# Kernel tuning notes

Measured on AMD Instinct MI355X. Metric: run time of the kernel, lower is better.

## Reference

```python
import jax, jax.numpy as jnp
import numpy as np

VX, VY = 0.16, 0.16
PC_RANGE = (0.0, -39.68, -3.0, 69.12, 39.68, 1.0)
X_OFFSET = VX / 2.0 + PC_RANGE[0]
Y_OFFSET = VY / 2.0 + PC_RANGE[1]
BN_EPS = 1e-3


def setup_inputs() -> dict:
    key = jax.random.key(0)
    k1, k2, k3, k4, k5, k6 = jax.random.split(key, 6)
    P, N, C_IN, C_AUG, C_OUT = 30000, 32, 4, 9, 64
    inputs = jax.random.normal(k1, (P, N, C_IN), dtype=jnp.float32)
    num_points = jnp.maximum(jax.random.randint(k2, (P,), 0, N, dtype=jnp.int32), 1)
    coords = jax.random.randint(k3, (P, 4), 0, 432, dtype=jnp.int32)
    # PFN layer params: Linear(9->64, no bias), BatchNorm1d(64) affine params
    W = jax.random.normal(k4, (C_AUG, C_OUT), dtype=jnp.float32) * (1.0 / np.sqrt(C_AUG))
    gamma = jnp.ones((C_OUT,), dtype=jnp.float32) + 0.1 * jax.random.normal(k5, (C_OUT,), dtype=jnp.float32)
    beta = 0.1 * jax.random.normal(k6, (C_OUT,), dtype=jnp.float32)
    return {"inputs": inputs, "num_points": num_points, "coords": coords,
            "W": W, "gamma": gamma, "beta": beta}


def reference(inputs, num_points, coords, W, gamma, beta):
    # inputs: (P, N, 4); num_points: (P,); coords: (P, 4) = (batch, z, y, x)
    P, N, _ = inputs.shape
    dtype = inputs.dtype
    npf = num_points.astype(dtype)

    # cluster offsets: per-pillar mean of xyz (sum over all N slots / num_points, as in source)
    points_mean = inputs[:, :, :3].sum(axis=1, keepdims=True) / npf[:, None, None]
    f_cluster = inputs[:, :, :3] - points_mean  # (P, N, 3)

    # center offsets w.r.t. pillar center
    cx = coords[:, 3].astype(dtype)[:, None] * VX + X_OFFSET  # (P, 1)
    cy = coords[:, 2].astype(dtype)[:, None] * VY + Y_OFFSET
    f_center = jnp.stack([inputs[:, :, 0] - cx, inputs[:, :, 1] - cy], axis=-1)  # (P, N, 2)

    feats = jnp.concatenate([inputs, f_cluster, f_center], axis=-1)  # (P, N, 9)

    # zero out padding points
    mask = (jnp.arange(N)[None, :] < num_points[:, None]).astype(dtype)[:, :, None]
    feats = feats * mask

    # PFNLayer: linear -> BatchNorm1d (training-mode batch stats over P*N) -> ReLU -> max over points
    x = jnp.einsum('pnc,cd->pnd', feats, W)  # (P, N, 64)
    mean = x.mean(axis=(0, 1))
    var = jnp.mean(jnp.square(x - mean), axis=(0, 1))  # biased, as torch BN
    x = (x - mean) * jax.lax.rsqrt(var + BN_EPS) * gamma + beta
    x = jax.nn.relu(x)
    return x.max(axis=1)  # (P, 64)
```

## Files before the change

### kernel.cpp

```cpp
#include <hip/hip_runtime.h>
#include <math.h>


#define NSLOT 32
#define NCH 64

static constexpr float kVX = 0.16f, kVY = 0.16f;
static constexpr float kXOff = 0.08f;
static constexpr float kYOff = 0.08f - 39.68f;
static constexpr float kEps = 1e-3f;
static constexpr float kNegInf = -3.402823466e38f;

typedef int sv16 __attribute__((ext_vector_type(16)));
typedef int sv8 __attribute__((ext_vector_type(8)));
union U16 { sv16 v; float f[16]; };
union U8  { sv8 v;  float f[8]; int i[8]; };

__device__ __forceinline__ const float* uptr(const float* p) {
    unsigned long long v = (unsigned long long)p;
    unsigned lo = __builtin_amdgcn_readfirstlane((unsigned)v);
    unsigned hi = __builtin_amdgcn_readfirstlane((unsigned)(v >> 32));
    return (const float*)(((unsigned long long)hi << 32) | lo);
}

__global__ __launch_bounds__(256) void k_stats(const float* __restrict__ in,
                                               const int* __restrict__ npts,
                                               const int* __restrict__ coords,
                                               float* __restrict__ part,
                                               float* __restrict__ meta, int P) {
    const int tid = threadIdx.x;
    const int lane = tid & 63;
    const int wv = tid >> 6;
    const int sub = lane & 3;
    const int pi = blockIdx.x * 64 + wv * 16 + (lane >> 2);
    const bool valid = pi < P;

    float T0 = 0.f, T1 = 0.f, T2 = 0.f;
    float S0 = 0.f, S1 = 0.f, S2 = 0.f, S3 = 0.f;
    float Q[10];
#pragma unroll
    for (int i = 0; i < 10; ++i) Q[i] = 0.f;
    float cx = 0.f, cy = 0.f, npf = 1.f;
    int np = 1;

    if (valid) {
        np = npts[pi];
        np = np < 1 ? 1 : (np > NSLOT ? NSLOT : np);
        npf = (float)np;
        const int4 cd = *reinterpret_cast<const int4*>(coords + (size_t)pi * 4);
        cx = (float)cd.w * kVX + kXOff;
        cy = (float)cd.z * kVY + kYOff;
        const float* bp = in + (size_t)pi * 128 + sub * 4;
#pragma unroll
        for (int k = 0; k < 8; ++k) {
            const float4 u = *reinterpret_cast<const float4*>(bp + k * 16);
            const int slot = sub + k * 4;
            T0 += u.x; T1 += u.y; T2 += u.z;
            const bool m = slot < np;
            const float ax = m ? u.x : 0.f, ay = m ? u.y : 0.f;
            const float az = m ? u.z : 0.f, aw = m ? u.w : 0.f;
            S0 += ax; S1 += ay; S2 += az; S3 += aw;
            Q[0] += ax * u.x; Q[1] += ax * u.y; Q[2] += ax * u.z; Q[3] += ax * u.w;
            Q[4] += ay * u.y; Q[5] += ay * u.z; Q[6] += ay * u.w;
            Q[7] += az * u.z; Q[8] += az * u.w;
            Q[9] += aw * u.w;
        }
    }

#define QUADR(v) { v += __shfl_xor(v, 1); v += __shfl_xor(v, 2); }
    QUADR(T0) QUADR(T1) QUADR(T2)
    QUADR(S0) QUADR(S1) QUADR(S2) QUADR(S3)
#pragma unroll
    for (int i = 0; i < 10; ++i) QUADR(Q[i])
#undef QUADR

    float acc[54];
#pragma unroll
    for (int i = 0; i < 54; ++i) acc[i] = 0.f;

    if (valid && sub == 0) {
        const float inv = 1.0f / npf;
        const float mx = T0 * inv, my = T1 * inv, mz = T2 * inv;
        if (meta) {
            *reinterpret_cast<float4*>(meta + (size_t)pi * 8) =
                make_float4(mx, my, mz, __int_as_float(np));
            *reinterpret_cast<float4*>(meta + (size_t)pi * 8 + 4) =
                make_float4(cx, cy, 0.f, 0.f);
        }
        const float AS[9] = {S0, S1, S2, S3, S0, S1, S2, S0, S1};
        const float b9[9] = {0.f, 0.f, 0.f, 0.f, -mx, -my, -mz, -cx, -cy};
        const int r9[9] = {0, 1, 2, 3, 0, 1, 2, 0, 1};
        float Qm[4][4];
        Qm[0][0] = Q[0]; Qm[0][1] = Q[1]; Qm[0][2] = Q[2]; Qm[0][3] = Q[3];
        Qm[1][0] = Q[1]; Qm[1][1] = Q[4]; Qm[1][2] = Q[5]; Qm[1][3] = Q[6];
        Qm[2][0] = Q[2]; Qm[2][1] = Q[5]; Qm[2][2] = Q[7]; Qm[2][3] = Q[8];
        Qm[3][0] = Q[3]; Qm[3][1] = Q[6]; Qm[3][2] = Q[8]; Qm[3][3] = Q[9];
#pragma unroll
        for (int i = 0; i < 9; ++i) acc[i] = AS[i] + npf * b9[i];
        int k = 9;
#pragma unroll
        for (int i = 0; i < 9; ++i)
#pragma unroll
            for (int j = i; j < 9; ++j) {
                acc[k] = Qm[r9[i]][r9[j]] + AS[i] * b9[j] + b9[i] * AS[j]
                         + npf * b9[i] * b9[j];
                ++k;
            }
    }

#pragma unroll
    for (int i = 0; i < 54; ++i) {
        acc[i] += __shfl_xor(acc[i], 4);
        acc[i] += __shfl_xor(acc[i], 8);
        acc[i] += __shfl_xor(acc[i], 16);
        acc[i] += __shfl_xor(acc[i], 32);
    }

    __shared__ float red[4][54];
    if (lane == 0) {
#pragma unroll
        for (int i = 0; i < 54; ++i) red[wv][i] = acc[i];
    }
    __syncthreads();
    if (tid < 54) {
        part[(size_t)blockIdx.x * 64 + tid] =
            red[0][tid] + red[1][tid] + red[2][tid] + red[3][tid];
    }
}

__global__ __launch_bounds__(1024) void k_mid(const float* __restrict__ part,
                                              const float* __restrict__ W,
                                              const float* __restrict__ gamma,
                                              const float* __restrict__ beta,
                                              float* __restrict__ fold,
                                              int nb, int P) {
    __shared__ float sred[16][64];
    __shared__ float ssum[64];
    const int tid = threadIdx.x;
    const int e = tid & 63;
    const int grp = tid >> 6;
    float v0 = 0.f, v1 = 0.f, v2 = 0.f, v3 = 0.f;
    int i = grp;
    for (; i + 48 < nb; i += 64) {
        v0 += part[(size_t)i * 64 + e];
        v1 += part[(size_t)(i + 16) * 64 + e];
        v2 += part[(size_t)(i + 32) * 64 + e];
        v3 += part[(size_t)(i + 48) * 64 + e];
    }
    for (; i < nb; i += 16) v0 += part[(size_t)i * 64 + e];
    sred[grp][e] = (v0 + v1) + (v2 + v3);
    __syncthreads();
    if (tid < 64) {
        float v = 0.f;
#pragma unroll
        for (int g = 0; g < 16; ++g) v += sred[g][tid];
        ssum[tid] = v;
    }
    __syncthreads();

    if (tid < 64) {
        const int d = tid;
        float Wc[9];
#pragma unroll
        for (int c = 0; c < 9; ++c) Wc[c] = W[c * NCH + d];
        const float invPN = 1.0f / ((float)P * (float)NSLOT);
        float mean = 0.f;
#pragma unroll
        for (int c = 0; c < 9; ++c) mean += ssum[c] * Wc[c];
        mean *= invPN;
        float e2 = 0.f;
        int k = 9;
#pragma unroll
        for (int i2 = 0; i2 < 9; ++i2)
#pragma unroll
            for (int j = i2; j < 9; ++j) {
                const float coef = (i2 == j) ? 1.f : 2.f;
                e2 += coef * ssum[k] * Wc[i2] * Wc[j];
                ++k;
            }
        e2 *= invPN;
        const float var = e2 - mean * mean;
        const float s = gamma[d] * rsqrtf(var + kEps);
        const float t = beta[d] - mean * s;
        fold[0 * 64 + d] = s * (Wc[0] + Wc[4] + Wc[7]);
        fold[1 * 64 + d] = s * (Wc[1] + Wc[5] + Wc[8]);
        fold[2 * 64 + d] = s * (Wc[2] + Wc[6]);
        fold[3 * 64 + d] = s * Wc[3];
        fold[4 * 64 + d] = s * Wc[4];
        fold[5 * 64 + d] = s * Wc[5];
        fold[6 * 64 + d] = s * Wc[6];
        fold[7 * 64 + d] = s * Wc[7];
        fold[8 * 64 + d] = s * Wc[8];
        fold[9 * 64 + d] = t;
    }
}

__device__ __forceinline__ float dot4(const float4 u, float V0, float V1,
                                      float V2, float V3, float c0) {
    return fmaf(u.x, V0, fmaf(u.y, V1, fmaf(u.z, V2, fmaf(u.w, V3, c0))));
}

template <bool MEANS>
__global__ __launch_bounds__(256) void k_out(const float* __restrict__ in,
                                             const int* __restrict__ npts,
                                             const int* __restrict__ coords,
                                             const float* __restrict__ fold,
                                             const float* __restrict__ meta,
                                             float* __restrict__ out, int P) {
    const int tid = threadIdx.x;
    const int lane = tid & 63;
    const int wv = tid >> 6;
    const int gwave = blockIdx.x * 4 + wv;
    const int nwave = gridDim.x * 4;

    float F[10];
#pragma unroll
    for (int j = 0; j < 10; ++j) F[j] = fold[j * 64 + lane];
    const float V0 = F[0], V1 = F[1], V2 = F[2], V3 = F[3];
    const float sW4 = F[4], sW5 = F[5], sW6 = F[6], sW7 = F[7], sW8 = F[8];
    const float t = F[9];

    if (MEANS) {
        for (int p = gwave; p < P; p += nwave) {
            const float* up = uptr(in + (size_t)p * 128);
            const float* mp = uptr(meta + (size_t)p * 8);
            U8 m; U16 g0, g1, g2, g3;
            asm volatile(
                "s_load_dwordx8 %0, %2, 0x0\n\t"
                "s_load_dwordx16 %1, %3, 0x0"
                : "=s"(m.v), "=s"(g0.v) : "s"(mp), "s"(up));
            asm volatile(
                "s_load_dwordx16 %0, %2, 0x40\n\t"
                "s_load_dwordx16 %1, %2, 0x80"
                : "=s"(g1.v), "=s"(g2.v) : "s"(up));
            asm volatile(
                "s_load_dwordx16 %0, %1, 0xc0"
                : "=s"(g3.v) : "s"(up));
            asm volatile("s_waitcnt lgkmcnt(0)" ::: "memory");
            __builtin_amdgcn_sched_barrier(0);

            const int np = m.i[3];
            const float c0 = t - fmaf(m.f[0], sW4, fmaf(m.f[1], sW5,
                                 fmaf(m.f[2], sW6, fmaf(m.f[4], sW7,
                                      m.f[5] * sW8))));
            float y0 = t, y1 = t, y2 = t, y3 = t;
#define SLOT4(G, B) { \
            const float z0 = fmaf(G.f[0], V0, fmaf(G.f[1], V1, \
                               fmaf(G.f[2], V2, fmaf(G.f[3], V3, c0)))); \
            const float z1 = fmaf(G.f[4], V0, fmaf(G.f[5], V1, \
                               fmaf(G.f[6], V2, fmaf(G.f[7], V3, c0)))); \
            const float z2 = fmaf(G.f[8], V0, fmaf(G.f[9], V1, \
                               fmaf(G.f[10], V2, fmaf(G.f[11], V3, c0)))); \
            const float z3 = fmaf(G.f[12], V0, fmaf(G.f[13], V1, \
                               fmaf(G.f[14], V2, fmaf(G.f[15], V3, c0)))); \
            y0 = fmaxf(y0, ((B) + 0 < np) ? z0 : t); \
            y1 = fmaxf(y1, ((B) + 1 < np) ? z1 : t); \
            y2 = fmaxf(y2, ((B) + 2 < np) ? z2 : t); \
            y3 = fmaxf(y3, ((B) + 3 < np) ? z3 : t); }

            SLOT4(g0, 0)
            SLOT4(g1, 4)
            if (np > 8) {
                SLOT4(g2, 8)
                SLOT4(g3, 12)
            }
            if (np > 16) {
                U16 h0, h1, h2, h3;
                asm volatile(
                    "s_load_dwordx16 %0, %2, 0x100\n\t"
                    "s_load_dwordx16 %1, %2, 0x140"
                    : "=s"(h0.v), "=s"(h1.v) : "s"(up));
                asm volatile(
                    "s_load_dwordx16 %0, %2, 0x180\n\t"
                    "s_load_dwordx16 %1, %2, 0x1c0"
                    : "=s"(h2.v), "=s"(h3.v) : "s"(up));
                asm volatile("s_waitcnt lgkmcnt(0)" ::: "memory");
                __builtin_amdgcn_sched_barrier(0);
                SLOT4(h0, 16)
                SLOT4(h1, 20)
                SLOT4(h2, 24)
                SLOT4(h3, 28)
            }
#undef SLOT4
            out[(size_t)p * NCH + lane] =
                fmaxf(fmaxf(fmaxf(y0, y1), fmaxf(y2, y3)), 0.f);
        }
    } else {
        __shared__ float lds[4][128];
        for (int p = gwave; p < P; p += nwave) {
            const float2 g = *reinterpret_cast<const float2*>(in + (size_t)p * 128 + lane * 2);
            int np = npts[p];
            np = np < 1 ? 1 : (np > NSLOT ? NSLOT : np);
            const bool ev = !(lane & 1);
            float px = ev ? g.x : 0.f;
            float py = ev ? g.y : 0.f;
            float pz = ev ? 0.f : g.x;
#pragma unroll
            for (int m = 1; m < 64; m <<= 1) {
                px += __shfl_xor(px, m);
                py += __shfl_xor(py, m);
                pz += __shfl_xor(pz, m);
            }
            const float npf = (float)np;
            const float mx = px / npf, my = py / npf, mz = pz / npf;
            const int4 cd = *reinterpret_cast<const int4*>(coords + (size_t)p * 4);
            const float cx = (float)cd.w * kVX + kXOff;
            const float cy = (float)cd.z * kVY + kYOff;
            const float c0 = t - (mx * sW4 + my * sW5 + mz * sW6 + cx * sW7 + cy * sW8);
            *reinterpret_cast<float2*>(&lds[wv][lane * 2]) = g;
            const float* L = lds[wv];
            float y0 = (np < NSLOT) ? t : kNegInf;
            float y1 = kNegInf;
            int n = 0;
            for (; n + 2 <= np; n += 2) {
                const float4 u0 = *reinterpret_cast<const float4*>(L + n * 4);
                const float4 u1 = *reinterpret_cast<const float4*>(L + n * 4 + 4);
                y0 = fmaxf(y0, dot4(u0, V0, V1, V2, V3, c0));
                y1 = fmaxf(y1, dot4(u1, V0, V1, V2, V3, c0));
            }
            if (n < np) {
                const float4 u0 = *reinterpret_cast<const float4*>(L + n * 4);
                y0 = fmaxf(y0, dot4(u0, V0, V1, V2, V3, c0));
            }
            out[(size_t)p * NCH + lane] = fmaxf(fmaxf(y0, y1), 0.f);
        }
    }
}

extern "C" void kernel_launch(void* const* d_in, const int* in_sizes, int n_in,
                              void* d_out, int out_size, void* d_ws, size_t ws_size,
                              hipStream_t stream) {
    const float* in = (const float*)d_in[0];
    const int* npts = (const int*)d_in[1];
    const int* coords = (const int*)d_in[2];
    const float* W = (const float*)d_in[3];
    const float* gamma = (const float*)d_in[4];
    const float* beta = (const float*)d_in[5];
    float* out = (float*)d_out;
    float* ws = (float*)d_ws;
    const int P = in_sizes[1];

    const int nb = (P + 63) / 64;
    const size_t foff = (size_t)nb * 64;
    const size_t moff = (foff + 640 + 63) & ~(size_t)63;
    float* part = ws;
    float* fold = ws + foff;
    const bool means = ws_size >= (moff + 8 * (size_t)P) * sizeof(float);
    float* meta = means ? (ws + moff) : nullptr;

    k_stats<<<nb, 256, 0, stream>>>(in, npts, coords, part, meta, P);
    k_mid<<<1, 1024, 0, stream>>>(part, W, gamma, beta, fold, nb, P);
    if (means) {
        k_out<true><<<2048, 256, 0, stream>>>(in, npts, coords, fold, meta, out, P);
    } else {
        k_out<false><<<2048, 256, 0, stream>>>(in, npts, coords, fold, meta, out, P);
    }
}
```

Before: 31.29 us.

## Fuse stats reduction into output kernel, dropping the single-block mid kernel

Removes the separate single-block k_mid launch. Each output block now redundantly reduces all partial statistics itself and folds the BatchNorm scale and shift into per-channel weights. The output grid changes from 2048 persistent blocks to one block per 32 pillars, and the LDS fallback path without meta is removed. This saves one launch and the serial single-block gap, but every one of about 938 blocks rereads the full part buffer (about 120 KB), adding redundant L2 traffic and latency before each block's main loop.

```diff
diff --git a/kernel.cpp b/kernel.cpp
--- a/kernel.cpp
+++ b/kernel.cpp
@@ -9,7 +9,6 @@
 static constexpr float kXOff = 0.08f;
 static constexpr float kYOff = 0.08f - 39.68f;
 static constexpr float kEps = 1e-3f;
-static constexpr float kNegInf = -3.402823466e38f;
 
 typedef int sv16 __attribute__((ext_vector_type(16)));
 typedef int sv8 __attribute__((ext_vector_type(8)));
@@ -81,12 +80,10 @@
     if (valid && sub == 0) {
         const float inv = 1.0f / npf;
         const float mx = T0 * inv, my = T1 * inv, mz = T2 * inv;
-        if (meta) {
-            *reinterpret_cast<float4*>(meta + (size_t)pi * 8) =
-                make_float4(mx, my, mz, __int_as_float(np));
-            *reinterpret_cast<float4*>(meta + (size_t)pi * 8 + 4) =
-                make_float4(cx, cy, 0.f, 0.f);
-        }
+        *reinterpret_cast<float4*>(meta + (size_t)pi * 8) =
+            make_float4(mx, my, mz, __int_as_float(np));
+        *reinterpret_cast<float4*>(meta + (size_t)pi * 8 + 4) =
+            make_float4(cx, cy, 0.f, 0.f);
         const float AS[9] = {S0, S1, S2, S3, S0, S1, S2, S0, S1};
         const float b9[9] = {0.f, 0.f, 0.f, 0.f, -mx, -my, -mz, -cx, -cy};
         const int r9[9] = {0, 1, 2, 3, 0, 1, 2, 0, 1};
@@ -128,47 +125,58 @@
     }
 }
 
-__global__ __launch_bounds__(1024) void k_mid(const float* __restrict__ part,
-                                              const float* __restrict__ W,
-                                              const float* __restrict__ gamma,
-                                              const float* __restrict__ beta,
-                                              float* __restrict__ fold,
-                                              int nb, int P) {
-    __shared__ float sred[16][64];
+__global__ __launch_bounds__(256) void k_out(const float* __restrict__ in,
+                                             const float* __restrict__ W,
+                                             const float* __restrict__ gamma,
+                                             const float* __restrict__ beta,
+                                             const float* __restrict__ part,
+                                             const float* __restrict__ meta,
+                                             float* __restrict__ out,
+                                             int P, int nb) {
+    __shared__ float sred[4][64];
     __shared__ float ssum[64];
     const int tid = threadIdx.x;
-    const int e = tid & 63;
-    const int grp = tid >> 6;
-    float v0 = 0.f, v1 = 0.f, v2 = 0.f, v3 = 0.f;
-    int i = grp;
-    for (; i + 48 < nb; i += 64) {
-        v0 += part[(size_t)i * 64 + e];
-        v1 += part[(size_t)(i + 16) * 64 + e];
-        v2 += part[(size_t)(i + 32) * 64 + e];
-        v3 += part[(size_t)(i + 48) * 64 + e];
-    }
-    for (; i < nb; i += 16) v0 += part[(size_t)i * 64 + e];
-    sred[grp][e] = (v0 + v1) + (v2 + v3);
-    __syncthreads();
-    if (tid < 64) {
-        float v = 0.f;
-#pragma unroll
-        for (int g = 0; g < 16; ++g) v += sred[g][tid];
-        ssum[tid] = v;
-    }
-    __syncthreads();
-
-    if (tid < 64) {
-        const int d = tid;
-        float Wc[9];
-#pragma unroll
-        for (int c = 0; c < 9; ++c) Wc[c] = W[c * NCH + d];
-        const float invPN = 1.0f / ((float)P * (float)NSLOT);
-        float mean = 0.f;
-#pragma unroll
-        for (int c = 0; c < 9; ++c) mean += ssum[c] * Wc[c];
-        mean *= invPN;
-        float e2 = 0.f;
+    const int lane = tid & 63;
+    const int wv = tid >> 6;
+
+    {
+        const int e = tid & 63;
+        const int grp = tid >> 6;
+        const int rpc = (nb + 3) >> 2;
+        const int i0 = grp * rpc;
+        const int i1 = min(i0 + rpc, nb);
+        float v0 = 0.f, v1 = 0.f, v2 = 0.f, v3 = 0.f;
+        float v4 = 0.f, v5 = 0.f, v6 = 0.f, v7 = 0.f;
+        int i = i0;
+        for (; i + 8 <= i1; i += 8) {
+            v0 += part[(size_t)(i + 0) * 64 + e];
+            v1 += part[(size_t)(i + 1) * 64 + e];
+            v2 += part[(size_t)(i + 2) * 64 + e];
+            v3 += part[(size_t)(i + 3) * 64 + e];
+            v4 += part[(size_t)(i + 4) * 64 + e];
+            v5 += part[(size_t)(i + 5) * 64 + e];
+            v6 += part[(size_t)(i + 6) * 64 + e];
+            v7 += part[(size_t)(i + 7) * 64 + e];
+        }
+        for (; i < i1; ++i) v0 += part[(size_t)i * 64 + e];
+        sred[grp][e] = ((v0 + v1) + (v2 + v3)) + ((v4 + v5) + (v6 + v7));
+        __syncthreads();
+        if (tid < 64)
+            ssum[tid] = sred[0][tid] + sred[1][tid] + sred[2][tid] + sred[3][tid];
+        __syncthreads();
+    }
+
+    const int d = lane;
+    float Wc[9];
+#pragma unroll
+    for (int c = 0; c < 9; ++c) Wc[c] = W[c * NCH + d];
+    const float invPN = 1.0f / ((float)P * (float)NSLOT);
+    float mean = 0.f;
+#pragma unroll
+    for (int c = 0; c < 9; ++c) mean += ssum[c] * Wc[c];
+    mean *= invPN;
+    float e2 = 0.f;
+    {
         int k = 9;
 #pragma unroll
         for (int i2 = 0; i2 < 9; ++i2)
@@ -178,152 +186,84 @@
                 e2 += coef * ssum[k] * Wc[i2] * Wc[j];
                 ++k;
             }
-        e2 *= invPN;
-        const float var = e2 - mean * mean;
-        const float s = gamma[d] * rsqrtf(var + kEps);
-        const float t = beta[d] - mean * s;
-        fold[0 * 64 + d] = s * (Wc[0] + Wc[4] + Wc[7]);
-        fold[1 * 64 + d] = s * (Wc[1] + Wc[5] + Wc[8]);
-        fold[2 * 64 + d] = s * (Wc[2] + Wc[6]);
-        fold[3 * 64 + d] = s * Wc[3];
-        fold[4 * 64 + d] = s * Wc[4];
-        fold[5 * 64 + d] = s * Wc[5];
-        fold[6 * 64 + d] = s * Wc[6];
-        fold[7 * 64 + d] = s * Wc[7];
-        fold[8 * 64 + d] = s * Wc[8];
-        fold[9 * 64 + d] = t;
-    }
-}
-
-__device__ __forceinline__ float dot4(const float4 u, float V0, float V1,
-                                      float V2, float V3, float c0) {
-    return fmaf(u.x, V0, fmaf(u.y, V1, fmaf(u.z, V2, fmaf(u.w, V3, c0))));
-}
-
-template <bool MEANS>
-__global__ __launch_bounds__(256) void k_out(const float* __restrict__ in,
-                                             const int* __restrict__ npts,
-                                             const int* __restrict__ coords,
-                                             const float* __restrict__ fold,
-                                             const float* __restrict__ meta,
-                                             float* __restrict__ out, int P) {
-    const int tid = threadIdx.x;
-    const int lane = tid & 63;
-    const int wv = tid >> 6;
-    const int gwave = blockIdx.x * 4 + wv;
-    const int nwave = gridDim.x * 4;
-
-    float F[10];
-#pragma unroll
-    for (int j = 0; j < 10; ++j) F[j] = fold[j * 64 + lane];
-    const float V0 = F[0], V1 = F[1], V2 = F[2], V3 = F[3];
-    const float sW4 = F[4], sW5 = F[5], sW6 = F[6], sW7 = F[7], sW8 = F[8];
-    const float t = F[9];
-
-    if (MEANS) {
-        for (int p = gwave; p < P; p += nwave) {
-            const float* up = uptr(in + (size_t)p * 128);
-            const float* mp = uptr(meta + (size_t)p * 8);
-            U8 m; U16 g0, g1, g2, g3;
+    }
+    e2 *= invPN;
+    const float var = e2 - mean * mean;
+    const float s = gamma[d] * rsqrtf(var + kEps);
+    const float t = beta[d] - mean * s;
+    const float V0 = s * (Wc[0] + Wc[4] + Wc[7]);
+    const float V1 = s * (Wc[1] + Wc[5] + Wc[8]);
+    const float V2 = s * (Wc[2] + Wc[6]);
+    const float V3 = s * Wc[3];
+    const float sW4 = s * Wc[4], sW5 = s * Wc[5], sW6 = s * Wc[6];
+    const float sW7 = s * Wc[7], sW8 = s * Wc[8];
+
+    const int p0 = blockIdx.x * 32;
+    const int qmax = min(32, P - p0);
+    for (int q = wv; q < qmax; q += 4) {
+        const int p = p0 + q;
+        const float* up = uptr(in + (size_t)p * 128);
+        const float* mp = uptr(meta + (size_t)p * 8);
+        U8 m; U16 g0, g1, g2, g3;
+        asm volatile(
+            "s_load_dwordx8 %0, %2, 0x0\n\t"
+            "s_load_dwordx16 %1, %3, 0x0"
+            : "=s"(m.v), "=s"(g0.v) : "s"(mp), "s"(up));
+        asm volatile(
+            "s_load_dwordx16 %0, %2, 0x40\n\t"
+            "s_load_dwordx16 %1, %2, 0x80"
+            : "=s"(g1.v), "=s"(g2.v) : "s"(up));
+        asm volatile(
+            "s_load_dwordx16 %0, %1, 0xc0"
+            : "=s"(g3.v) : "s"(up));
+        asm volatile("s_waitcnt lgkmcnt(0)" ::: "memory");
+        __builtin_amdgcn_sched_barrier(0);
+
+        const int np = m.i[3];
+        const float c0 = t - fmaf(m.f[0], sW4, fmaf(m.f[1], sW5,
+                             fmaf(m.f[2], sW6, fmaf(m.f[4], sW7,
+                                  m.f[5] * sW8))));
+        float y0 = t, y1 = t, y2 = t, y3 = t;
+#define SLOT4(G, B) { \
+        const float z0 = fmaf(G.f[0], V0, fmaf(G.f[1], V1, \
+                           fmaf(G.f[2], V2, fmaf(G.f[3], V3, c0)))); \
+        const float z1 = fmaf(G.f[4], V0, fmaf(G.f[5], V1, \
+                           fmaf(G.f[6], V2, fmaf(G.f[7], V3, c0)))); \
+        const float z2 = fmaf(G.f[8], V0, fmaf(G.f[9], V1, \
+                           fmaf(G.f[10], V2, fmaf(G.f[11], V3, c0)))); \
+        const float z3 = fmaf(G.f[12], V0, fmaf(G.f[13], V1, \
+                           fmaf(G.f[14], V2, fmaf(G.f[15], V3, c0)))); \
+        y0 = fmaxf(y0, ((B) + 0 < np) ? z0 : t); \
+        y1 = fmaxf(y1, ((B) + 1 < np) ? z1 : t); \
+        y2 = fmaxf(y2, ((B) + 2 < np) ? z2 : t); \
+        y3 = fmaxf(y3, ((B) + 3 < np) ? z3 : t); }
+
+        SLOT4(g0, 0)
+        SLOT4(g1, 4)
+        if (np > 8) {
+            SLOT4(g2, 8)
+            SLOT4(g3, 12)
+        }
+        if (np > 16) {
+            U16 h0, h1, h2, h3;
             asm volatile(
-                "s_load_dwordx8 %0, %2, 0x0\n\t"
-                "s_load_dwordx16 %1, %3, 0x0"
-                : "=s"(m.v), "=s"(g0.v) : "s"(mp), "s"(up));
+                "s_load_dwordx16 %0, %2, 0x100\n\t"
+                "s_load_dwordx16 %1, %2, 0x140"
+                : "=s"(h0.v), "=s"(h1.v) : "s"(up));
             asm volatile(
-                "s_load_dwordx16 %0, %2, 0x40\n\t"
-                "s_load_dwordx16 %1, %2, 0x80"
-                : "=s"(g1.v), "=s"(g2.v) : "s"(up));
-            asm volatile(
-                "s_load_dwordx16 %0, %1, 0xc0"
-                : "=s"(g3.v) : "s"(up));
+                "s_load_dwordx16 %0, %2, 0x180\n\t"
+                "s_load_dwordx16 %1, %2, 0x1c0"
+                : "=s"(h2.v), "=s"(h3.v) : "s"(up));
             asm volatile("s_waitcnt lgkmcnt(0)" ::: "memory");
             __builtin_amdgcn_sched_barrier(0);
-
-            const int np = m.i[3];
-            const float c0 = t - fmaf(m.f[0], sW4, fmaf(m.f[1], sW5,
-                                 fmaf(m.f[2], sW6, fmaf(m.f[4], sW7,
-                                      m.f[5] * sW8))));
-            float y0 = t, y1 = t, y2 = t, y3 = t;
-#define SLOT4(G, B) { \
-            const float z0 = fmaf(G.f[0], V0, fmaf(G.f[1], V1, \
-                               fmaf(G.f[2], V2, fmaf(G.f[3], V3, c0)))); \
-            const float z1 = fmaf(G.f[4], V0, fmaf(G.f[5], V1, \
-                               fmaf(G.f[6], V2, fmaf(G.f[7], V3, c0)))); \
-            const float z2 = fmaf(G.f[8], V0, fmaf(G.f[9], V1, \
-                               fmaf(G.f[10], V2, fmaf(G.f[11], V3, c0)))); \
-            const float z3 = fmaf(G.f[12], V0, fmaf(G.f[13], V1, \
-                               fmaf(G.f[14], V2, fmaf(G.f[15], V3, c0)))); \
-            y0 = fmaxf(y0, ((B) + 0 < np) ? z0 : t); \
-            y1 = fmaxf(y1, ((B) + 1 < np) ? z1 : t); \
-            y2 = fmaxf(y2, ((B) + 2 < np) ? z2 : t); \
-            y3 = fmaxf(y3, ((B) + 3 < np) ? z3 : t); }
-
-            SLOT4(g0, 0)
-            SLOT4(g1, 4)
-            if (np > 8) {
-                SLOT4(g2, 8)
-                SLOT4(g3, 12)
-            }
-            if (np > 16) {
-                U16 h0, h1, h2, h3;
-                asm volatile(
-                    "s_load_dwordx16 %0, %2, 0x100\n\t"
-                    "s_load_dwordx16 %1, %2, 0x140"
-                    : "=s"(h0.v), "=s"(h1.v) : "s"(up));
-                asm volatile(
-                    "s_load_dwordx16 %0, %2, 0x180\n\t"
-                    "s_load_dwordx16 %1, %2, 0x1c0"
-                    : "=s"(h2.v), "=s"(h3.v) : "s"(up));
-                asm volatile("s_waitcnt lgkmcnt(0)" ::: "memory");
-                __builtin_amdgcn_sched_barrier(0);
-                SLOT4(h0, 16)
-                SLOT4(h1, 20)
-                SLOT4(h2, 24)
-                SLOT4(h3, 28)
-            }
+            SLOT4(h0, 16)
+            SLOT4(h1, 20)
+            SLOT4(h2, 24)
+            SLOT4(h3, 28)
+        }
 #undef SLOT4
-            out[(size_t)p * NCH + lane] =
-                fmaxf(fmaxf(fmaxf(y0, y1), fmaxf(y2, y3)), 0.f);
-        }
-    } else {
-        __shared__ float lds[4][128];
-        for (int p = gwave; p < P; p += nwave) {
-            const float2 g = *reinterpret_cast<const float2*>(in + (size_t)p * 128 + lane * 2);
-            int np = npts[p];
-            np = np < 1 ? 1 : (np > NSLOT ? NSLOT : np);
-            const bool ev = !(lane & 1);
-            float px = ev ? g.x : 0.f;
-            float py = ev ? g.y : 0.f;
-            float pz = ev ? 0.f : g.x;
-#pragma unroll
-            for (int m = 1; m < 64; m <<= 1) {
-                px += __shfl_xor(px, m);
-                py += __shfl_xor(py, m);
-                pz += __shfl_xor(pz, m);
-            }
-            const float npf = (float)np;
-            const float mx = px / npf, my = py / npf, mz = pz / npf;
-            const int4 cd = *reinterpret_cast<const int4*>(coords + (size_t)p * 4);
-            const float cx = (float)cd.w * kVX + kXOff;
-            const float cy = (float)cd.z * kVY + kYOff;
-            const float c0 = t - (mx * sW4 + my * sW5 + mz * sW6 + cx * sW7 + cy * sW8);
-            *reinterpret_cast<float2*>(&lds[wv][lane * 2]) = g;
-            const float* L = lds[wv];
-            float y0 = (np < NSLOT) ? t : kNegInf;
-            float y1 = kNegInf;
-            int n = 0;
-            for (; n + 2 <= np; n += 2) {
-                const float4 u0 = *reinterpret_cast<const float4*>(L + n * 4);
-                const float4 u1 = *reinterpret_cast<const float4*>(L + n * 4 + 4);
-                y0 = fmaxf(y0, dot4(u0, V0, V1, V2, V3, c0));
-                y1 = fmaxf(y1, dot4(u1, V0, V1, V2, V3, c0));
-            }
-            if (n < np) {
-                const float4 u0 = *reinterpret_cast<const float4*>(L + n * 4);
-                y0 = fmaxf(y0, dot4(u0, V0, V1, V2, V3, c0));
-            }
-            out[(size_t)p * NCH + lane] = fmaxf(fmaxf(y0, y1), 0.f);
-        }
+        out[(size_t)p * NCH + lane] =
+            fmaxf(fmaxf(fmaxf(y0, y1), fmaxf(y2, y3)), 0.f);
     }
 }
 
@@ -341,18 +281,11 @@
     const int P = in_sizes[1];
 
     const int nb = (P + 63) / 64;
-    const size_t foff = (size_t)nb * 64;
-    const size_t moff = (foff + 640 + 63) & ~(size_t)63;
+    const size_t moff = ((size_t)nb * 64 + 63) & ~(size_t)63;
     float* part = ws;
-    float* fold = ws + foff;
-    const bool means = ws_size >= (moff + 8 * (size_t)P) * sizeof(float);
-    float* meta = means ? (ws + moff) : nullptr;
+    float* meta = ws + moff;
 
     k_stats<<<nb, 256, 0, stream>>>(in, npts, coords, part, meta, P);
-    k_mid<<<1, 1024, 0, stream>>>(part, W, gamma, beta, fold, nb, P);
-    if (means) {
-        k_out<true><<<2048, 256, 0, stream>>>(in, npts, coords, fold, meta, out, P);
-    } else {
-        k_out<false><<<2048, 256, 0, stream>>>(in, npts, coords, fold, meta, out, P);
-    }
-}
+    const int ob = (P + 31) / 32;
+    k_out<<<ob, 256, 0, stream>>>(in, W, gamma, beta, part, meta, out, P, nb);
+}
```

After: 35.66 us. 1.14x slower.

## Replace shuffle reduction with LDS transpose and specialize slot masking

Applied to the files above, without the earlier changes.

In k_stats, the 54-value cross-lane shuffle reduction is replaced by writing each pillar's accumulators to a padded LDS matrix and summing columns across threads. In k_out, the fallback non-meta path is removed, so the meta workspace is always assumed present. Groups of four slots that are fully valid now skip the per-slot np comparison and select, and partial groups past np are skipped. This trims shuffle traffic and ALU selects, at the cost of more LDS use and branchier code, and it no longer checks that the workspace is large enough.

```diff
diff --git a/kernel.cpp b/kernel.cpp
--- a/kernel.cpp
+++ b/kernel.cpp
@@ -9,7 +9,6 @@
 static constexpr float kXOff = 0.08f;
 static constexpr float kYOff = 0.08f - 39.68f;
 static constexpr float kEps = 1e-3f;
-static constexpr float kNegInf = -3.402823466e38f;
 
 typedef int sv16 __attribute__((ext_vector_type(16)));
 typedef int sv8 __attribute__((ext_vector_type(8)));
@@ -28,6 +27,8 @@
                                                const int* __restrict__ coords,
                                                float* __restrict__ part,
                                                float* __restrict__ meta, int P) {
+    __shared__ float Rm[64][57];
+    __shared__ float s2[4][54];
     const int tid = threadIdx.x;
     const int lane = tid & 63;
     const int wv = tid >> 6;
@@ -81,12 +82,10 @@
     if (valid && sub == 0) {
         const float inv = 1.0f / npf;
         const float mx = T0 * inv, my = T1 * inv, mz = T2 * inv;
-        if (meta) {
-            *reinterpret_cast<float4*>(meta + (size_t)pi * 8) =
-                make_float4(mx, my, mz, __int_as_float(np));
-            *reinterpret_cast<float4*>(meta + (size_t)pi * 8 + 4) =
-                make_float4(cx, cy, 0.f, 0.f);
-        }
+        *reinterpret_cast<float4*>(meta + (size_t)pi * 8) =
+            make_float4(mx, my, mz, __int_as_float(np));
+        *reinterpret_cast<float4*>(meta + (size_t)pi * 8 + 4) =
+            make_float4(cx, cy, 0.f, 0.f);
         const float AS[9] = {S0, S1, S2, S3, S0, S1, S2, S0, S1};
         const float b9[9] = {0.f, 0.f, 0.f, 0.f, -mx, -my, -mz, -cx, -cy};
         const int r9[9] = {0, 1, 2, 3, 0, 1, 2, 0, 1};
@@ -108,23 +107,28 @@
             }
     }
 
-#pragma unroll
-    for (int i = 0; i < 54; ++i) {
-        acc[i] += __shfl_xor(acc[i], 4);
-        acc[i] += __shfl_xor(acc[i], 8);
-        acc[i] += __shfl_xor(acc[i], 16);
-        acc[i] += __shfl_xor(acc[i], 32);
-    }
-
-    __shared__ float red[4][54];
-    if (lane == 0) {
-#pragma unroll
-        for (int i = 0; i < 54; ++i) red[wv][i] = acc[i];
+    {
+        const int q = wv * 16 + (lane >> 2);
+        if (sub == 0) {
+#pragma unroll
+            for (int e = 0; e < 54; ++e) Rm[q][e] = acc[e];
+        }
+    }
+    __syncthreads();
+    {
+        const int e = tid & 63;
+        const int g = tid >> 6;
+        if (e < 54) {
+            float v = 0.f;
+#pragma unroll
+            for (int r = 0; r < 16; ++r) v += Rm[g * 16 + r][e];
+            s2[g][e] = v;
+        }
     }
     __syncthreads();
     if (tid < 54) {
         part[(size_t)blockIdx.x * 64 + tid] =
-            red[0][tid] + red[1][tid] + red[2][tid] + red[3][tid];
+            s2[0][tid] + s2[1][tid] + s2[2][tid] + s2[3][tid];
     }
 }
 
@@ -195,15 +199,7 @@
     }
 }
 
-__device__ __forceinline__ float dot4(const float4 u, float V0, float V1,
-                                      float V2, float V3, float c0) {
-    return fmaf(u.x, V0, fmaf(u.y, V1, fmaf(u.z, V2, fmaf(u.w, V3, c0))));
-}
-
-template <bool MEANS>
 __global__ __launch_bounds__(256) void k_out(const float* __restrict__ in,
-                                             const int* __restrict__ npts,
-                                             const int* __restrict__ coords,
                                              const float* __restrict__ fold,
                                              const float* __restrict__ meta,
                                              float* __restrict__ out, int P) {
@@ -220,110 +216,77 @@
     const float sW4 = F[4], sW5 = F[5], sW6 = F[6], sW7 = F[7], sW8 = F[8];
     const float t = F[9];
 
-    if (MEANS) {
-        for (int p = gwave; p < P; p += nwave) {
-            const float* up = uptr(in + (size_t)p * 128);
-            const float* mp = uptr(meta + (size_t)p * 8);
-            U8 m; U16 g0, g1, g2, g3;
+    for (int p = gwave; p < P; p += nwave) {
+        const float* up = uptr(in + (size_t)p * 128);
+        const float* mp = uptr(meta + (size_t)p * 8);
+        U8 m; U16 g0, g1, g2, g3;
+        asm volatile(
+            "s_load_dwordx8 %0, %2, 0x0\n\t"
+            "s_load_dwordx16 %1, %3, 0x0"
+            : "=s"(m.v), "=s"(g0.v) : "s"(mp), "s"(up));
+        asm volatile(
+            "s_load_dwordx16 %0, %2, 0x40\n\t"
+            "s_load_dwordx16 %1, %2, 0x80"
+            : "=s"(g1.v), "=s"(g2.v) : "s"(up));
+        asm volatile(
+            "s_load_dwordx16 %0, %1, 0xc0"
+            : "=s"(g3.v) : "s"(up));
+        asm volatile("s_waitcnt lgkmcnt(0)" ::: "memory");
+        __builtin_amdgcn_sched_barrier(0);
+
+        const int np = m.i[3];
+        const float c0 = t - fmaf(m.f[0], sW4, fmaf(m.f[1], sW5,
+                             fmaf(m.f[2], sW6, fmaf(m.f[4], sW7,
+                                  m.f[5] * sW8))));
+        float y0 = t, y1 = t, y2 = t, y3 = t;
+#define Z4(G) \
+        const float z0 = fmaf(G.f[0], V0, fmaf(G.f[1], V1, \
+                           fmaf(G.f[2], V2, fmaf(G.f[3], V3, c0)))); \
+        const float z1 = fmaf(G.f[4], V0, fmaf(G.f[5], V1, \
+                           fmaf(G.f[6], V2, fmaf(G.f[7], V3, c0)))); \
+        const float z2 = fmaf(G.f[8], V0, fmaf(G.f[9], V1, \
+                           fmaf(G.f[10], V2, fmaf(G.f[11], V3, c0)))); \
+        const float z3 = fmaf(G.f[12], V0, fmaf(G.f[13], V1, \
+                           fmaf(G.f[14], V2, fmaf(G.f[15], V3, c0))));
+#define SLOT4F(G) { Z4(G) \
+        y0 = fmaxf(y0, z0); y1 = fmaxf(y1, z1); \
+        y2 = fmaxf(y2, z2); y3 = fmaxf(y3, z3); }
+#define SLOT4P(G, B) { Z4(G) \
+        y0 = fmaxf(y0, ((B) + 0 < np) ? z0 : t); \
+        y1 = fmaxf(y1, ((B) + 1 < np) ? z1 : t); \
+        y2 = fmaxf(y2, ((B) + 2 < np) ? z2 : t); \
+        y3 = fmaxf(y3, ((B) + 3 < np) ? z3 : t); }
+
+        if (np >= 8) { SLOT4F(g0) SLOT4F(g1) }
+        else { SLOT4P(g0, 0) if (np > 4) SLOT4P(g1, 4) }
+        if (np > 8) {
+            if (np >= 16) { SLOT4F(g2) SLOT4F(g3) }
+            else { SLOT4P(g2, 8) if (np > 12) SLOT4P(g3, 12) }
+        }
+        if (np > 16) {
+            U16 h0, h1, h2, h3;
             asm volatile(
-                "s_load_dwordx8 %0, %2, 0x0\n\t"
-                "s_load_dwordx16 %1, %3, 0x0"
-                : "=s"(m.v), "=s"(g0.v) : "s"(mp), "s"(up));
+                "s_load_dwordx16 %0, %2, 0x100\n\t"
+                "s_load_dwordx16 %1, %2, 0x140"
+                : "=s"(h0.v), "=s"(h1.v) : "s"(up));
             asm volatile(
-                "s_load_dwordx16 %0, %2, 0x40\n\t"
-                "s_load_dwordx16 %1, %2, 0x80"
-                : "=s"(g1.v), "=s"(g2.v) : "s"(up));
-            asm volatile(
-                "s_load_dwordx16 %0, %1, 0xc0"
-                : "=s"(g3.v) : "s"(up));
+                "s_load_dwordx16 %0, %2, 0x180\n\t"
+                "s_load_dwordx16 %1, %2, 0x1c0"
+                : "=s"(h2.v), "=s"(h3.v) : "s"(up));
             asm volatile("s_waitcnt lgkmcnt(0)" ::: "memory");
             __builtin_amdgcn_sched_barrier(0);
-
-            const int np = m.i[3];
-            const float c0 = t - fmaf(m.f[0], sW4, fmaf(m.f[1], sW5,
-                                 fmaf(m.f[2], sW6, fmaf(m.f[4], sW7,
-                                      m.f[5] * sW8))));
-            float y0 = t, y1 = t, y2 = t, y3 = t;
-#define SLOT4(G, B) { \
-            const float z0 = fmaf(G.f[0], V0, fmaf(G.f[1], V1, \
-                               fmaf(G.f[2], V2, fmaf(G.f[3], V3, c0)))); \
-            const float z1 = fmaf(G.f[4], V0, fmaf(G.f[5], V1, \
-                               fmaf(G.f[6], V2, fmaf(G.f[7], V3, c0)))); \
-            const float z2 = fmaf(G.f[8], V0, fmaf(G.f[9], V1, \
-                               fmaf(G.f[10], V2, fmaf(G.f[11], V3, c0)))); \
-            const float z3 = fmaf(G.f[12], V0, fmaf(G.f[13], V1, \
-                               fmaf(G.f[14], V2, fmaf(G.f[15], V3, c0)))); \
-            y0 = fmaxf(y0, ((B) + 0 < np) ? z0 : t); \
-            y1 = fmaxf(y1, ((B) + 1 < np) ? z1 : t); \
-            y2 = fmaxf(y2, ((B) + 2 < np) ? z2 : t); \
-            y3 = fmaxf(y3, ((B) + 3 < np) ? z3 : t); }
-
-            SLOT4(g0, 0)
-            SLOT4(g1, 4)
-            if (np > 8) {
-                SLOT4(g2, 8)
-                SLOT4(g3, 12)
+            if (np >= 24) { SLOT4F(h0) SLOT4F(h1) }
+            else { SLOT4P(h0, 16) if (np > 20) SLOT4P(h1, 20) }
+            if (np > 24) {
+                if (np >= 28) { SLOT4F(h2) if (np > 28) SLOT4P(h3, 28) }
+                else { SLOT4P(h2, 24) }
             }
-            if (np > 16) {
-                U16 h0, h1, h2, h3;
-                asm volatile(
-                    "s_load_dwordx16 %0, %2, 0x100\n\t"
-                    "s_load_dwordx16 %1, %2, 0x140"
-                    : "=s"(h0.v), "=s"(h1.v) : "s"(up));
-                asm volatile(
-                    "s_load_dwordx16 %0, %2, 0x180\n\t"
-                    "s_load_dwordx16 %1, %2, 0x1c0"
-                    : "=s"(h2.v), "=s"(h3.v) : "s"(up));
-                asm volatile("s_waitcnt lgkmcnt(0)" ::: "memory");
-                __builtin_amdgcn_sched_barrier(0);
-                SLOT4(h0, 16)
-                SLOT4(h1, 20)
-                SLOT4(h2, 24)
-                SLOT4(h3, 28)
-            }
-#undef SLOT4
-            out[(size_t)p * NCH + lane] =
-                fmaxf(fmaxf(fmaxf(y0, y1), fmaxf(y2, y3)), 0.f);
-        }
-    } else {
-        __shared__ float lds[4][128];
-        for (int p = gwave; p < P; p += nwave) {
-            const float2 g = *reinterpret_cast<const float2*>(in + (size_t)p * 128 + lane * 2);
-            int np = npts[p];
-            np = np < 1 ? 1 : (np > NSLOT ? NSLOT : np);
-            const bool ev = !(lane & 1);
-            float px = ev ? g.x : 0.f;
-            float py = ev ? g.y : 0.f;
-            float pz = ev ? 0.f : g.x;
-#pragma unroll
-            for (int m = 1; m < 64; m <<= 1) {
-                px += __shfl_xor(px, m);
-                py += __shfl_xor(py, m);
-                pz += __shfl_xor(pz, m);
-            }
-            const float npf = (float)np;
-            const float mx = px / npf, my = py / npf, mz = pz / npf;
-            const int4 cd = *reinterpret_cast<const int4*>(coords + (size_t)p * 4);
-            const float cx = (float)cd.w * kVX + kXOff;
-            const float cy = (float)cd.z * kVY + kYOff;
-            const float c0 = t - (mx * sW4 + my * sW5 + mz * sW6 + cx * sW7 + cy * sW8);
-            *reinterpret_cast<float2*>(&lds[wv][lane * 2]) = g;
-            const float* L = lds[wv];
-            float y0 = (np < NSLOT) ? t : kNegInf;
-            float y1 = kNegInf;
-            int n = 0;
-            for (; n + 2 <= np; n += 2) {
-                const float4 u0 = *reinterpret_cast<const float4*>(L + n * 4);
-                const float4 u1 = *reinterpret_cast<const float4*>(L + n * 4 + 4);
-                y0 = fmaxf(y0, dot4(u0, V0, V1, V2, V3, c0));
-                y1 = fmaxf(y1, dot4(u1, V0, V1, V2, V3, c0));
-            }
-            if (n < np) {
-                const float4 u0 = *reinterpret_cast<const float4*>(L + n * 4);
-                y0 = fmaxf(y0, dot4(u0, V0, V1, V2, V3, c0));
-            }
-            out[(size_t)p * NCH + lane] = fmaxf(fmaxf(y0, y1), 0.f);
-        }
+        }
+#undef SLOT4F
+#undef SLOT4P
+#undef Z4
+        out[(size_t)p * NCH + lane] =
+            fmaxf(fmaxf(fmaxf(y0, y1), fmaxf(y2, y3)), 0.f);
     }
 }
 
@@ -345,14 +308,9 @@
     const size_t moff = (foff + 640 + 63) & ~(size_t)63;
     float* part = ws;
     float* fold = ws + foff;
-    const bool means = ws_size >= (moff + 8 * (size_t)P) * sizeof(float);
-    float* meta = means ? (ws + moff) : nullptr;
+    float* meta = ws + moff;
 
     k_stats<<<nb, 256, 0, stream>>>(in, npts, coords, part, meta, P);
     k_mid<<<1, 1024, 0, stream>>>(part, W, gamma, beta, fold, nb, P);
-    if (means) {
-        k_out<true><<<2048, 256, 0, stream>>>(in, npts, coords, fold, meta, out, P);
-    } else {
-        k_out<false><<<2048, 256, 0, stream>>>(in, npts, coords, fold, meta, out, P);
-    }
-}
+    k_out<<<2048, 256, 0, stream>>>(in, fold, meta, out, P);
+}
```

After: 39.18 us. 1.25x slower.
